# Kernel optimization log

Hardware: AMD Instinct MI355X
Metric: run time of the kernel (lower is better)

The kernel has to match this reference:

```python
import math
import jax, jax.numpy as jnp
import numpy as np

B, S, D, H = 4, 2048, 768, 12
HD = D // H  # 64


def setup_inputs() -> dict:
    key = jax.random.key(0)
    ks = jax.random.split(key, 10)
    sc = 0.02
    return {
        "hidden_states": jax.random.normal(ks[0], (B, S, D), dtype=jnp.float32),
        "attention_mask": jax.random.randint(ks[1], (1, H, S, S), 0, 2).astype(jnp.bool_),
        "q_w": jax.random.normal(ks[2], (D, D), dtype=jnp.float32) * sc,
        "q_b": jax.random.normal(ks[3], (D,), dtype=jnp.float32) * sc,
        "k_w": jax.random.normal(ks[4], (D, D), dtype=jnp.float32) * sc,
        "k_b": jax.random.normal(ks[5], (D,), dtype=jnp.float32) * sc,
        "v_w": jax.random.normal(ks[6], (D, D), dtype=jnp.float32) * sc,
        "v_b": jax.random.normal(ks[7], (D,), dtype=jnp.float32) * sc,
        "out_w": jax.random.normal(ks[8], (D, D), dtype=jnp.float32) * sc,
        "out_b": jax.random.normal(ks[9], (D,), dtype=jnp.float32) * sc,
    }


def _split_heads(x):
    # [B, S, D] -> [B, H, S, HD]
    b, s, _ = x.shape
    return x.reshape(b, s, H, HD).transpose(0, 2, 1, 3)


def reference(hidden_states, attention_mask, q_w, q_b, k_w, k_b, v_w, v_b, out_w, out_b):
    q = _split_heads(hidden_states @ q_w.T + q_b)
    k = _split_heads(hidden_states @ k_w.T + k_b)
    v = _split_heads(hidden_states @ v_w.T + v_b)
    scores = jnp.einsum("bhqd,bhkd->bhqk", q, k) / math.sqrt(HD)
    # prune_mode, before softmax: masked_fill(~mask, -inf)
    scores = jnp.where(attention_mask, scores, -jnp.inf)
    probs = jax.nn.softmax(scores, axis=-1)  # [B, H, S, S]
    ctx = jnp.einsum("bhqk,bhkd->bhqd", probs, v)
    ctx = ctx.transpose(0, 2, 1, 3).reshape(hidden_states.shape[0], -1, D)
    return ctx @ out_w.T + out_b
```

## Files before the change

### kernel.cpp

```cpp
#include <hip/hip_runtime.h>
#include <hip/hip_bf16.h>

#define B_ 4
#define S_ 2048
#define D_ 768
#define H_ 12
#define HD_ 64

typedef __attribute__((ext_vector_type(8))) short bf16x8;
typedef __attribute__((ext_vector_type(4))) float floatx4;

#define QSCALE 0.18033688011112042f

__device__ __forceinline__ unsigned short f2bf(float x) {
    union { float f; unsigned int u; } v; v.f = x;
    unsigned int r = v.u + 0x7fffu + ((v.u >> 16) & 1u);
    return (unsigned short)(r >> 16);
}

__device__ __forceinline__ unsigned int pk2bf(float a, float b) {
    __hip_bfloat162 h = __float22bfloat162_rn(make_float2(a, b));
    unsigned int u;
    __builtin_memcpy(&u, &h, 4);
    return u;
}

__device__ __forceinline__ void gload_lds16(const void* g, void* l) {
    __builtin_amdgcn_global_load_lds(
        (const __attribute__((address_space(1))) unsigned int*)g,
        (__attribute__((address_space(3))) unsigned int*)l, 16, 0, 0);
}

__device__ __forceinline__ bf16x8 ld_b64x2(const unsigned short* p) {
    union { bf16x8 v; unsigned long long q[2]; } u;
    u.q[0] = *(const unsigned long long*)p;
    u.q[1] = *(const unsigned long long*)(p + 4);
    return u.v;
}

__global__ void prep(const float* __restrict__ hs,
                     const float* __restrict__ w0, const float* __restrict__ w1,
                     const float* __restrict__ w2, const float* __restrict__ w3,
                     const int* __restrict__ mask,
                     unsigned short* __restrict__ Xb,
                     unsigned short* __restrict__ Wb,
                     unsigned long long* __restrict__ bits) {
    int bid = blockIdx.x;
    int t = threadIdx.x;
    if (bid < 6144) {
        int i = bid * 256 + t;
        float4 f = ((const float4*)hs)[i];
        ushort4 o;
        o.x = f2bf(f.x); o.y = f2bf(f.y); o.z = f2bf(f.z); o.w = f2bf(f.w);
        ((ushort4*)Xb)[i] = o;
    } else if (bid < 8448) {
        int q = bid - 6144;
        int wid = q / 576;
        const float* src = (wid == 0) ? w0 : (wid == 1) ? w1 : (wid == 2) ? w2 : w3;
        unsigned short* d = Wb + (size_t)wid * 589824;
        int i = (q - wid * 576) * 256 + t;
        float4 f = ((const float4*)src)[i];
        ushort4 o;
        o.x = f2bf(f.x); o.y = f2bf(f.y); o.z = f2bf(f.z); o.w = f2bf(f.w);
        ((ushort4*)d)[i] = o;
    } else {
        int q = bid - 8448;
        int lane = t & 63, wv = t >> 6;
#pragma unroll
        for (int j = 0; j < 8; j++) {
            size_t gw = (size_t)q * 32 + j * 4 + wv;
            size_t base = gw * 256;
            unsigned long long b0 = __ballot(mask[base + lane] != 0);
            unsigned long long b1 = __ballot(mask[base + 64 + lane] != 0);
            unsigned long long b2 = __ballot(mask[base + 128 + lane] != 0);
            unsigned long long b3 = __ballot(mask[base + 192 + lane] != 0);
            if (lane == 0) {
                bits[gw * 4 + 0] = b0; bits[gw * 4 + 1] = b1;
                bits[gw * 4 + 2] = b2; bits[gw * 4 + 3] = b3;
            }
        }
    }
}

__global__ __launch_bounds__(256) void qkv_gemm(
    const unsigned short* __restrict__ Xb,
    const unsigned short* __restrict__ Wq, const unsigned short* __restrict__ Wk,
    const unsigned short* __restrict__ Wv,
    const float* __restrict__ bq, const float* __restrict__ bk,
    const float* __restrict__ bv,
    unsigned short* __restrict__ Qo, unsigned short* __restrict__ Ko,
    unsigned short* __restrict__ Vo)
{
    const int lin = blockIdx.x + 64 * (blockIdx.y + 6 * blockIdx.z);
    const int nn = (lin & 7) * 144 + (lin >> 3);
    const int z = nn % 3;
    const int xy = nn / 3;
    const int m0 = (xy & 63) * 128;
    const int n0 = (xy >> 6) * 128;

    const unsigned short* W = (z == 0) ? Wq : (z == 1) ? Wk : Wv;
    const float* bias = (z == 0) ? bq : (z == 1) ? bk : bv;
    unsigned short* Out = (z == 0) ? Qo : (z == 1) ? Ko : Vo;
    const float scale = (z == 0) ? QSCALE : 1.0f;

    __shared__ alignas(16) unsigned short SMall[16384];
    unsigned short* SM = SMall;

    const int t = threadIdx.x;
    const int lane = t & 63, w = t >> 6;
    const int c = lane & 15, quad = lane >> 4;
    const int wm = (w & 1) * 64, wn = (w >> 1) * 64;

    const int srowq = lane >> 2, sc8 = (lane & 3) * 8;

    floatx4 acc[4][4];
#pragma unroll
    for (int i = 0; i < 4; i++)
#pragma unroll
        for (int j = 0; j < 4; j++) acc[i][j] = (floatx4){0.f, 0.f, 0.f, 0.f};

#pragma unroll
    for (int i = 0; i < 2; i++) {
        int chunk = i * 4 + w;
        int row = chunk * 16 + srowq;
        gload_lds16(&Xb[(size_t)(m0 + row) * 768 + sc8], &SMall[chunk * 512]);
        gload_lds16(&W [(size_t)(n0 + row) * 768 + sc8], &SMall[4096 + chunk * 512]);
    }

    for (int it = 0; it < 24; it++) {
        const int cur = it & 1;
        __syncthreads();
        if (it + 1 < 24) {
            int k1 = (it + 1) * 32;
#pragma unroll
            for (int i = 0; i < 2; i++) {
                int chunk = i * 4 + w;
                int row = chunk * 16 + srowq;
                gload_lds16(&Xb[(size_t)(m0 + row) * 768 + k1 + sc8],
                            &SMall[(cur ^ 1) * 8192 + chunk * 512]);
                gload_lds16(&W [(size_t)(n0 + row) * 768 + k1 + sc8],
                            &SMall[(cur ^ 1) * 8192 + 4096 + chunk * 512]);
            }
        }
        const unsigned short* As = &SMall[cur * 8192];
        const unsigned short* Bs = As + 4096;
        bf16x8 a[4], b[4];
#pragma unroll
        for (int i = 0; i < 4; i++)
            a[i] = *(const bf16x8*)&As[(wm + i * 16 + c) * 32 + quad * 8];
#pragma unroll
        for (int j = 0; j < 4; j++)
            b[j] = *(const bf16x8*)&Bs[(wn + j * 16 + c) * 32 + quad * 8];
#pragma unroll
        for (int i = 0; i < 4; i++)
#pragma unroll
            for (int j = 0; j < 4; j++)
                acc[i][j] = __builtin_amdgcn_mfma_f32_16x16x32_bf16(
                    a[i], b[j], acc[i][j], 0, 0, 0);
    }
    __syncthreads();

    const int bb = m0 >> 11, ssb = m0 & 2047;
    if (z == 2) {
#pragma unroll
        for (int half = 0; half < 2; half++) {
            if ((w >> 1) == half) {
#pragma unroll
                for (int j = 0; j < 4; j++) {
                    int n_l = j * 16 + c;
                    float bias_n = bias[n0 + half * 64 + n_l];
#pragma unroll
                    for (int i = 0; i < 4; i++) {
#pragma unroll
                        for (int r = 0; r < 4; r++) {
                            int m = wm + i * 16 + quad * 4 + r;
                            int ms = m ^ (c << 3);
                            SM[n_l * 128 + ms] = f2bf(acc[i][j][r] + bias_n);
                        }
                    }
                }
            }
            __syncthreads();
#pragma unroll
            for (int rb = 0; rb < 2; rb++) {
                int n_l = (t >> 3) + rb * 32;
                int ch = t & 7;
                int n_abs = n0 + half * 64 + n_l;
                int hh = n_abs >> 6, dd = n_abs & 63;
                unsigned short* dst =
                    Out + (((size_t)(bb * H_ + hh)) * 64 + dd) * S_ + ssb;
#pragma unroll
                for (int p = 0; p < 2; p++) {
                    int mc = ch + p * 8;
                    uint4 v = *(const uint4*)&SM[n_l * 128 + ((mc ^ (n_l & 15)) * 8)];
                    *(uint4*)&dst[mc * 8] = v;
                }
            }
            __syncthreads();
        }
    } else {
#pragma unroll
        for (int half = 0; half < 2; half++) {
            if ((w >> 1) == half) {
#pragma unroll
                for (int j = 0; j < 4; j++) {
                    float bias_n = bias[n0 + half * 64 + j * 16 + c];
#pragma unroll
                    for (int i = 0; i < 4; i++) {
#pragma unroll
                        for (int r = 0; r < 4; r++) {
                            int m = wm + i * 16 + quad * 4 + r;
                            int chunk = (j * 2 + (c >> 3)) ^ ((m >> 1) & 7);
                            SM[m * 64 + chunk * 8 + (c & 7)] =
                                f2bf((acc[i][j][r] + bias_n) * scale);
                        }
                    }
                }
            }
            __syncthreads();
            {
                int hh = (n0 >> 6) + half;
                unsigned short* dst =
                    Out + ((size_t)(bb * H_ + hh) * S_ + ssb) * 64;
#pragma unroll
                for (int i = 0; i < 4; i++) {
                    int idx = i * 256 + t;
                    int m = idx >> 3, ch = idx & 7;
                    uint4 v = *(const uint4*)&SM[m * 64 + ((ch ^ ((m >> 1) & 7)) * 8)];
                    *(uint4*)&dst[(size_t)m * 64 + ch * 8] = v;
                }
            }
            __syncthreads();
        }
    }
}

__global__ __launch_bounds__(256) void out_gemm(
    const unsigned short* __restrict__ Cb, const unsigned short* __restrict__ Wo,
    const float* __restrict__ bo, float* __restrict__ out)
{
    const int lin = blockIdx.x + 128 * blockIdx.y;
    const int nn = (lin & 7) * 96 + (lin >> 3);
    const int m0 = (nn & 127) * 64;
    const int n0 = (nn >> 7) * 128;

    __shared__ alignas(16) unsigned short SMall[12288];

    const int t = threadIdx.x;
    const int lane = t & 63, w = t >> 6;
    const int c = lane & 15, quad = lane >> 4;
    const int wm = (w & 1) * 32, wn = (w >> 1) * 64;

    const int arow = w * 16 + (lane >> 2);
    const int brow0 = (lane >> 2);
    const int sc8 = (lane & 3) * 8;

    floatx4 acc[2][4];
#pragma unroll
    for (int i = 0; i < 2; i++)
#pragma unroll
        for (int j = 0; j < 4; j++) acc[i][j] = (floatx4){0.f, 0.f, 0.f, 0.f};

    gload_lds16(&Cb[(size_t)(m0 + arow) * 768 + sc8], &SMall[w * 512]);
#pragma unroll
    for (int i = 0; i < 2; i++) {
        int chunk = i * 4 + w;
        gload_lds16(&Wo[(size_t)(n0 + chunk * 16 + brow0) * 768 + sc8],
                    &SMall[2048 + chunk * 512]);
    }

    for (int it = 0; it < 24; it++) {
        const int cur = it & 1;
        __syncthreads();
        if (it + 1 < 24) {
            int k1 = (it + 1) * 32;
            gload_lds16(&Cb[(size_t)(m0 + arow) * 768 + k1 + sc8],
                        &SMall[(cur ^ 1) * 6144 + w * 512]);
#pragma unroll
            for (int i = 0; i < 2; i++) {
                int chunk = i * 4 + w;
                gload_lds16(&Wo[(size_t)(n0 + chunk * 16 + brow0) * 768 + k1 + sc8],
                            &SMall[(cur ^ 1) * 6144 + 2048 + chunk * 512]);
            }
        }
        const unsigned short* As = &SMall[cur * 6144];
        const unsigned short* Bs = As + 2048;
        bf16x8 a[2], b[4];
#pragma unroll
        for (int i = 0; i < 2; i++)
            a[i] = *(const bf16x8*)&As[(wm + i * 16 + c) * 32 + quad * 8];
#pragma unroll
        for (int j = 0; j < 4; j++)
            b[j] = *(const bf16x8*)&Bs[(wn + j * 16 + c) * 32 + quad * 8];
#pragma unroll
        for (int i = 0; i < 2; i++)
#pragma unroll
            for (int j = 0; j < 4; j++)
                acc[i][j] = __builtin_amdgcn_mfma_f32_16x16x32_bf16(
                    a[i], b[j], acc[i][j], 0, 0, 0);
    }
    __syncthreads();

    float* SMf = (float*)SMall;
#pragma unroll
    for (int qtr = 0; qtr < 4; qtr++) {
        if ((w >> 1) == (qtr >> 1)) {
#pragma unroll
            for (int jj = 0; jj < 2; jj++) {
                int j = (qtr & 1) * 2 + jj;
                float bias_n = bo[n0 + wn + j * 16 + c];
                int chunk = jj * 4 + (c >> 2);
#pragma unroll
                for (int i = 0; i < 2; i++) {
#pragma unroll
                    for (int r = 0; r < 4; r++) {
                        int m = wm + i * 16 + quad * 4 + r;
                        SMf[m * 32 + ((chunk ^ (m & 7)) * 4) + (c & 3)] =
                            acc[i][j][r] + bias_n;
                    }
                }
            }
        }
        __syncthreads();
#pragma unroll
        for (int i = 0; i < 2; i++) {
            int idx = i * 256 + t;
            int m = idx >> 3, ch = idx & 7;
            float4 v = *(const float4*)&SMf[m * 32 + ((ch ^ (m & 7)) * 4)];
            *(float4*)&out[(size_t)(m0 + m) * 768 + n0 + qtr * 32 + ch * 4] = v;
        }
        __syncthreads();
    }
}

__global__ __launch_bounds__(256) void attn(
    const unsigned short* __restrict__ Q, const unsigned short* __restrict__ K,
    const unsigned short* __restrict__ Vt,
    const unsigned long long* __restrict__ mbits,
    unsigned short* __restrict__ ctx)
{
    const int lin = blockIdx.y * 16 + blockIdx.x;
    const int nn = (lin & 7) * 96 + (lin >> 3);
    const int qt = nn & 15;
    const int bh = nn >> 4;
    const int b = bh / H_, h = bh % H_;

    const unsigned short* Qp = Q + (size_t)bh * S_ * 64 + (size_t)qt * 128 * 64;
    const unsigned short* Kp = K + (size_t)bh * S_ * 64;
    const unsigned short* Vp = Vt + (size_t)bh * 64 * S_;

    __shared__ alignas(16) unsigned short Ks[2][64 * 64];
    __shared__ alignas(16) unsigned short Vs[2][64 * 64];
    __shared__ alignas(16) unsigned short Ps[4][2][16 * 68];

    const int t = threadIdx.x;
    const int lane = t & 63, w = t >> 6;
    const int c = lane & 15, quad = lane >> 4;

    bf16x8 aq[2][2];
#pragma unroll
    for (int st = 0; st < 2; st++) {
        aq[st][0] = *(const bf16x8*)&Qp[(size_t)(w * 32 + st * 16 + c) * 64 + quad * 8];
        aq[st][1] = *(const bf16x8*)&Qp[(size_t)(w * 32 + st * 16 + c) * 64 + 32 + quad * 8];
    }

    const unsigned long long* mrow =
        mbits + ((size_t)h * S_ + qt * 128 + w * 32 + quad * 4) * (S_ / 64);

    floatx4 acc_o[2][4];
#pragma unroll
    for (int st = 0; st < 2; st++)
#pragma unroll
        for (int i = 0; i < 4; i++) acc_o[st][i] = (floatx4){0.f, 0.f, 0.f, 0.f};
    float lp[2][4] = {{0.f, 0.f, 0.f, 0.f}, {0.f, 0.f, 0.f, 0.f}};

    const int srow = (lane >> 3);
    const int rc0 = ((quad     ) ^ (c & 7)) * 8;
    const int rc1 = ((quad + 4) ^ (c & 7)) * 8;

#pragma unroll
    for (int i = 0; i < 2; i++) {
        int chunk = i * 4 + w;
        int row = chunk * 8 + srow;
        int col8 = (((lane & 7) ^ ((row >> 2) & 7))) * 8;
        gload_lds16(&Kp[(size_t)row * 64 + col8], &Ks[0][chunk * 512]);
        gload_lds16(&Vp[(size_t)row * S_ + col8], &Vs[0][chunk * 512]);
    }

    for (int kt = 0; kt < S_ / 64; kt++) {
        const int cur = kt & 1;
        __syncthreads();
        if (kt + 1 < S_ / 64) {
#pragma unroll
            for (int i = 0; i < 2; i++) {
                int chunk = i * 4 + w;
                int row = chunk * 8 + srow;
                int col8 = (((lane & 7) ^ ((row >> 2) & 7))) * 8;
                gload_lds16(&Kp[(size_t)((kt + 1) * 64 + row) * 64 + col8],
                            &Ks[cur ^ 1][chunk * 512]);
                gload_lds16(&Vp[(size_t)row * S_ + (kt + 1) * 64 + col8],
                            &Vs[cur ^ 1][chunk * 512]);
            }
        }

#pragma unroll
        for (int p = 0; p < 2; p++) {
            floatx4 zz[2][2];
            zz[0][0] = (floatx4){0.f, 0.f, 0.f, 0.f};
            zz[0][1] = (floatx4){0.f, 0.f, 0.f, 0.f};
            zz[1][0] = (floatx4){0.f, 0.f, 0.f, 0.f};
            zz[1][1] = (floatx4){0.f, 0.f, 0.f, 0.f};
#pragma unroll
            for (int q2 = 0; q2 < 2; q2++) {
                int kr = 4 * c + 2 * p + q2;
                bf16x8 bk0 = *(const bf16x8*)&Ks[cur][kr * 64 + rc0];
                bf16x8 bk1 = *(const bf16x8*)&Ks[cur][kr * 64 + rc1];
                zz[0][q2] = __builtin_amdgcn_mfma_f32_16x16x32_bf16(aq[0][0], bk0, zz[0][q2], 0, 0, 0);
                zz[0][q2] = __builtin_amdgcn_mfma_f32_16x16x32_bf16(aq[0][1], bk1, zz[0][q2], 0, 0, 0);
                zz[1][q2] = __builtin_amdgcn_mfma_f32_16x16x32_bf16(aq[1][0], bk0, zz[1][q2], 0, 0, 0);
                zz[1][q2] = __builtin_amdgcn_mfma_f32_16x16x32_bf16(aq[1][1], bk1, zz[1][q2], 0, 0, 0);
            }

            asm volatile("" ::: "memory");
#pragma unroll
            for (int st = 0; st < 2; st++) {
#pragma unroll
                for (int r = 0; r < 4; r++) {
                    unsigned int n2 =
                        (unsigned int)(mrow[st * 16 * (S_ / 64) + r * (S_ / 64) + kt]
                                       >> (4 * c + 2 * p)) & 3u;
                    float p0 = (n2 & 1u) ? __builtin_amdgcn_exp2f(zz[st][0][r]) : 0.f;
                    float p1 = (n2 & 2u) ? __builtin_amdgcn_exp2f(zz[st][1][r]) : 0.f;
                    lp[st][r] += p0 + p1;
                    *(unsigned int*)&Ps[w][st][(quad * 4 + r) * 68 + 4 * c + 2 * p] =
                        pk2bf(p0, p1);
                }
            }
            asm volatile("" ::: "memory");
        }

        bf16x8 ap[2][2];
#pragma unroll
        for (int st = 0; st < 2; st++) {
            ap[st][0] = ld_b64x2(&Ps[w][st][c * 68 + quad * 8]);
            ap[st][1] = ld_b64x2(&Ps[w][st][c * 68 + 32 + quad * 8]);
        }

#pragma unroll
        for (int nt = 0; nt < 4; nt++) {
            int vr = 4 * c + nt;
            bf16x8 bv0 = *(const bf16x8*)&Vs[cur][vr * 64 + rc0];
            bf16x8 bv1 = *(const bf16x8*)&Vs[cur][vr * 64 + rc1];
#pragma unroll
            for (int st = 0; st < 2; st++) {
                acc_o[st][nt] = __builtin_amdgcn_mfma_f32_16x16x32_bf16(ap[st][0], bv0, acc_o[st][nt], 0, 0, 0);
                acc_o[st][nt] = __builtin_amdgcn_mfma_f32_16x16x32_bf16(ap[st][1], bv1, acc_o[st][nt], 0, 0, 0);
            }
        }
    }

#pragma unroll
    for (int st = 0; st < 2; st++)
#pragma unroll
        for (int r = 0; r < 4; r++) {
            float s = lp[st][r];
#pragma unroll
            for (int o = 1; o < 16; o <<= 1) s += __shfl_xor(s, o, 64);
            lp[st][r] = s;
        }

#pragma unroll
    for (int st = 0; st < 2; st++)
#pragma unroll
        for (int nt = 0; nt < 4; nt++)
#pragma unroll
            for (int r = 0; r < 4; r++) {
                int qrow = qt * 128 + w * 32 + st * 16 + quad * 4 + r;
                int dd = 4 * c + nt;
                float v = acc_o[st][nt][r] / lp[st][r];
                ctx[((size_t)b * S_ + qrow) * 768 + h * 64 + dd] = f2bf(v);
            }
}

extern "C" void kernel_launch(void* const* d_in, const int* in_sizes, int n_in,
                              void* d_out, int out_size, void* d_ws, size_t ws_size,
                              hipStream_t stream) {
    const float* hs    = (const float*)d_in[0];
    const int*   mask  = (const int*)d_in[1];
    const float* q_w   = (const float*)d_in[2];
    const float* q_b   = (const float*)d_in[3];
    const float* k_w   = (const float*)d_in[4];
    const float* k_b   = (const float*)d_in[5];
    const float* v_w   = (const float*)d_in[6];
    const float* v_b   = (const float*)d_in[7];
    const float* out_w = (const float*)d_in[8];
    const float* out_b = (const float*)d_in[9];
    float* out = (float*)d_out;

    unsigned short* Xb  = (unsigned short*)d_ws;
    unsigned short* Wqb = Xb + 6291456;
    unsigned short* Wkb = Wqb + 589824;
    unsigned short* Wvb = Wkb + 589824;
    unsigned short* Wob = Wvb + 589824;
    unsigned short* Qb  = Wob + 589824;
    unsigned short* Kb  = Qb + 6291456;
    unsigned short* Vtb = Kb + 6291456;
    unsigned short* Cb  = Vtb + 6291456;
    unsigned long long* mbits = (unsigned long long*)(Cb + 6291456);

    prep<<<14592, 256, 0, stream>>>(hs, q_w, k_w, v_w, out_w, mask, Xb, Wqb, mbits);
    qkv_gemm<<<dim3(64, 6, 3), 256, 0, stream>>>(Xb, Wqb, Wkb, Wvb,
                                                 q_b, k_b, v_b, Qb, Kb, Vtb);
    attn<<<dim3(16, 48), 256, 0, stream>>>(Qb, Kb, Vtb, mbits, Cb);
    out_gemm<<<dim3(128, 6), 256, 0, stream>>>(Cb, Wob, out_b, out);
}
```

Baseline: 500.3 us.

## Simplify block mapping, flatten mask packing grid, hoist mask loads in attention

```diff
diff --git a/kernel.cpp b/kernel.cpp
--- a/kernel.cpp
+++ b/kernel.cpp
@@ -64,20 +64,16 @@
         o.x = f2bf(f.x); o.y = f2bf(f.y); o.z = f2bf(f.z); o.w = f2bf(f.w);
         ((ushort4*)d)[i] = o;
     } else {
-        int q = bid - 8448;
-        int lane = t & 63, wv = t >> 6;
-#pragma unroll
-        for (int j = 0; j < 8; j++) {
-            size_t gw = (size_t)q * 32 + j * 4 + wv;
-            size_t base = gw * 256;
-            unsigned long long b0 = __ballot(mask[base + lane] != 0);
-            unsigned long long b1 = __ballot(mask[base + 64 + lane] != 0);
-            unsigned long long b2 = __ballot(mask[base + 128 + lane] != 0);
-            unsigned long long b3 = __ballot(mask[base + 192 + lane] != 0);
-            if (lane == 0) {
-                bits[gw * 4 + 0] = b0; bits[gw * 4 + 1] = b1;
-                bits[gw * 4 + 2] = b2; bits[gw * 4 + 3] = b3;
-            }
+        size_t gw = ((size_t)(bid - 8448) * 256 + t) >> 6;
+        int lane = t & 63;
+        size_t base = gw * 256;
+        unsigned long long b0 = __ballot(mask[base + lane] != 0);
+        unsigned long long b1 = __ballot(mask[base + 64 + lane] != 0);
+        unsigned long long b2 = __ballot(mask[base + 128 + lane] != 0);
+        unsigned long long b3 = __ballot(mask[base + 192 + lane] != 0);
+        if (lane == 0) {
+            bits[gw * 4 + 0] = b0; bits[gw * 4 + 1] = b1;
+            bits[gw * 4 + 2] = b2; bits[gw * 4 + 3] = b3;
         }
     }
 }
@@ -91,17 +87,14 @@
     unsigned short* __restrict__ Qo, unsigned short* __restrict__ Ko,
     unsigned short* __restrict__ Vo)
 {
-    const int lin = blockIdx.x + 64 * (blockIdx.y + 6 * blockIdx.z);
-    const int nn = (lin & 7) * 144 + (lin >> 3);
-    const int z = nn % 3;
-    const int xy = nn / 3;
-    const int m0 = (xy & 63) * 128;
-    const int n0 = (xy >> 6) * 128;
-
+    const int z = blockIdx.z;
     const unsigned short* W = (z == 0) ? Wq : (z == 1) ? Wk : Wv;
     const float* bias = (z == 0) ? bq : (z == 1) ? bk : bv;
     unsigned short* Out = (z == 0) ? Qo : (z == 1) ? Ko : Vo;
     const float scale = (z == 0) ? QSCALE : 1.0f;
+
+    const int m0 = blockIdx.x * 128;
+    const int n0 = blockIdx.y * 128;
 
     __shared__ alignas(16) unsigned short SMall[16384];
     unsigned short* SM = SMall;
@@ -239,10 +232,8 @@
     const unsigned short* __restrict__ Cb, const unsigned short* __restrict__ Wo,
     const float* __restrict__ bo, float* __restrict__ out)
 {
-    const int lin = blockIdx.x + 128 * blockIdx.y;
-    const int nn = (lin & 7) * 96 + (lin >> 3);
-    const int m0 = (nn & 127) * 64;
-    const int n0 = (nn >> 7) * 128;
+    const int m0 = blockIdx.x * 64;
+    const int n0 = blockIdx.y * 128;
 
     __shared__ alignas(16) unsigned short SMall[12288];
 
@@ -390,6 +381,14 @@
     for (int kt = 0; kt < S_ / 64; kt++) {
         const int cur = kt & 1;
         __syncthreads();
+
+        unsigned long long mk[2][4];
+#pragma unroll
+        for (int st = 0; st < 2; st++)
+#pragma unroll
+            for (int r = 0; r < 4; r++)
+                mk[st][r] = mrow[st * 512 + r * 32 + kt];
+
         if (kt + 1 < S_ / 64) {
 #pragma unroll
             for (int i = 0; i < 2; i++) {
@@ -427,8 +426,7 @@
 #pragma unroll
                 for (int r = 0; r < 4; r++) {
                     unsigned int n2 =
-                        (unsigned int)(mrow[st * 16 * (S_ / 64) + r * (S_ / 64) + kt]
-                                       >> (4 * c + 2 * p)) & 3u;
+                        (unsigned int)(mk[st][r] >> (4 * c + 2 * p)) & 3u;
                     float p0 = (n2 & 1u) ? __builtin_amdgcn_exp2f(zz[st][0][r]) : 0.f;
                     float p1 = (n2 & 2u) ? __builtin_amdgcn_exp2f(zz[st][1][r]) : 0.f;
                     lp[st][r] += p0 + p1;
@@ -508,7 +506,7 @@
     unsigned short* Cb  = Vtb + 6291456;
     unsigned long long* mbits = (unsigned long long*)(Cb + 6291456);
 
-    prep<<<14592, 256, 0, stream>>>(hs, q_w, k_w, v_w, out_w, mask, Xb, Wqb, mbits);
+    prep<<<57600, 256, 0, stream>>>(hs, q_w, k_w, v_w, out_w, mask, Xb, Wqb, mbits);
     qkv_gemm<<<dim3(64, 6, 3), 256, 0, stream>>>(Xb, Wqb, Wkb, Wvb,
                                                  q_b, k_b, v_b, Qb, Kb, Vtb);
     attn<<<dim3(16, 48), 256, 0, stream>>>(Qb, Kb, Vtb, mbits, Cb);
```

Result: faster. 472.5 us (-5.6%).
